# Optimization experiments

Measured on AMD Instinct MI355X. Metric: run time of the kernel, lower is better.

Reference implementation:

```python
import jax, jax.numpy as jnp
import numpy as np

D_MODEL = 1024
NUM_HEADS = 16

def setup_inputs() -> dict:
    key = jax.random.key(0)
    ks = jax.random.split(key, 5)
    std = np.sqrt(2.0 / (D_MODEL + D_MODEL))
    def w(k):
        # trunc_normal approx: normal clipped to +-3 std
        v = jax.random.truncated_normal(k, -3.0, 3.0, (D_MODEL, D_MODEL), dtype=jnp.float32) * std
        return v
    return {
        "x": jax.random.normal(ks[0], (2, 2048, D_MODEL), dtype=jnp.float32),
        "w_q": w(ks[1]),
        "w_k": w(ks[2]),
        "w_v": w(ks[3]),
        "w_o": w(ks[4]),
    }

def reference(x, w_q, w_k, w_v, w_o):
    B, S, D = x.shape
    H = NUM_HEADS
    dk = D // H
    # Linear: y = x @ W^T  (weight is [d_out, d_in])
    def proj(w):
        y = jnp.einsum('bsd,ed->bse', x, w)
        return y.reshape(B, S, H, dk).transpose(0, 2, 1, 3)  # [B,H,S,dk]
    q, k, v = proj(w_q), proj(w_k), proj(w_v)
    scale = 1.0 / jnp.sqrt(jnp.float32(dk))
    scores = jnp.einsum('bhqd,bhkd->bhqk', q, k) * scale  # [B,H,S,S]
    causal = jnp.tril(jnp.ones((S, S), dtype=bool))
    scores = jnp.where(causal, scores, -jnp.inf)
    attn = jax.nn.softmax(scores, axis=-1)
    out = jnp.einsum('bhqk,bhkd->bhqd', attn, v)  # [B,H,S,dk]
    out = out.transpose(0, 2, 1, 3).reshape(B, S, D)
    return jnp.einsum('bsd,ed->bse', out, w_o)
```

## Files before the change

kernel.cpp:

```cpp
#include <hip/hip_runtime.h>
#include <hip/hip_bf16.h>
#include <stdint.h>

#define S_LEN 2048
#define DM    1024
#define NH    16
#define DK    64
#define NBATCH 2

typedef __attribute__((ext_vector_type(8))) short bf8_t;
typedef __attribute__((ext_vector_type(4))) short s4_t;
typedef __attribute__((ext_vector_type(4))) float f4_t;

using bf16 = __hip_bfloat16;

#define NEG_BIG (-1.0e30f)
#define SCALE2  (0.125f * 1.44269504088896f)

static __device__ __forceinline__ f4_t mfma16(bf8_t a, bf8_t b, f4_t c) {
    return __builtin_amdgcn_mfma_f32_16x16x32_bf16(a, b, c, 0, 0, 0);
}

static __device__ __forceinline__ short f2b(float f) {
    __hip_bfloat16 h = __float2bfloat16(f);
    return *reinterpret_cast<short*>(&h);
}

static __device__ __forceinline__ void g2l16(const bf16* g, bf16* l) {
#if __has_builtin(__builtin_amdgcn_global_load_lds)
    __builtin_amdgcn_global_load_lds(
        (const __attribute__((address_space(1))) void*)g,
        (__attribute__((address_space(3))) void*)l, 16, 0, 0);
#else
    *(bf8_t*)l = *(const bf8_t*)g;
#endif
}

__global__ __launch_bounds__(256)
void cvt_all(const float* __restrict__ x,  const float* __restrict__ wq,
             const float* __restrict__ wk, const float* __restrict__ wv,
             const float* __restrict__ wo, bf16* __restrict__ ob) {
    const size_t SEG = 1u << 20;
    size_t i = ((size_t)blockIdx.x * 256 + threadIdx.x) * 8;
    const float* src;
    if      (i < 4 * SEG) src = x  + i;
    else if (i < 5 * SEG) src = wq + (i - 4 * SEG);
    else if (i < 6 * SEG) src = wk + (i - 5 * SEG);
    else if (i < 7 * SEG) src = wv + (i - 6 * SEG);
    else                  src = wo + (i - 7 * SEG);
    float4 f0 = *(const float4*)(src);
    float4 f1 = *(const float4*)(src + 4);
    bf8_t v;
    v[0]=f2b(f0.x); v[1]=f2b(f0.y); v[2]=f2b(f0.z); v[3]=f2b(f0.w);
    v[4]=f2b(f1.x); v[5]=f2b(f1.y); v[6]=f2b(f1.z); v[7]=f2b(f1.w);
    *(bf8_t*)(ob + i) = v;
}

#define GEMM_B_MAINLOOP(Aptr, Bptr)                                          \
    __shared__ bf16 As[128][32];                                             \
    __shared__ bf16 Bs[128][32];                                             \
    const int tid  = threadIdx.x;                                            \
    const int lane = tid & 63;                                               \
    const int w    = tid >> 6;                                               \
    const int wr   = w >> 1, wc = w & 1;                                     \
    const int lhi  = lane >> 4, llo = lane & 15;                             \
    const int bm   = blockIdx.x * 128;                                       \
    const int bn   = blockIdx.y * 128;                                       \
    const int r0c  = tid >> 2;                           \
    const int c0c  = (tid & 3) << 3;                     \
    const int r1c  = (256 + tid) >> 2;                                       \
    f4_t acc[4][4] = {};                                                     \
    for (int k0 = 0; k0 < 1024; k0 += 32) {                                  \
        __syncthreads();                                                     \
        g2l16(Aptr + (size_t)(bm + r0c) * 1024 + k0 + c0c,                   \
              &As[0][0] + (size_t)tid * 8);                                  \
        g2l16(Aptr + (size_t)(bm + r1c) * 1024 + k0 + c0c,                   \
              &As[0][0] + (size_t)(256 + tid) * 8);                          \
        g2l16(Bptr + (size_t)(bn + r0c) * 1024 + k0 + c0c,                   \
              &Bs[0][0] + (size_t)tid * 8);                                  \
        g2l16(Bptr + (size_t)(bn + r1c) * 1024 + k0 + c0c,                   \
              &Bs[0][0] + (size_t)(256 + tid) * 8);                          \
        asm volatile("s_waitcnt vmcnt(0)" ::: "memory");                     \
        __syncthreads();                                                     \
        bf8_t af[4], bfr[4];                                                 \
        _Pragma("unroll")                                                    \
        for (int i = 0; i < 4; ++i) {                                        \
            af[i]  = *(const bf8_t*)(&As[wr * 64 + i * 16 + llo][lhi * 8]);  \
            bfr[i] = *(const bf8_t*)(&Bs[wc * 64 + i * 16 + llo][lhi * 8]);  \
        }                                                                    \
        _Pragma("unroll")                                                    \
        for (int mi = 0; mi < 4; ++mi)                                       \
            _Pragma("unroll")                                                \
            for (int ni = 0; ni < 4; ++ni)                                   \
                acc[mi][ni] = mfma16(af[mi], bfr[ni], acc[mi][ni]);          \
    }

__global__ __launch_bounds__(256)
void gemm_qkv_b(const bf16* __restrict__ xb,
                const bf16* __restrict__ wqb, const bf16* __restrict__ wkb,
                const bf16* __restrict__ wvb,
                bf16* __restrict__ qws, bf16* __restrict__ kws,
                bf16* __restrict__ vtws) {
    const int z = blockIdx.z;
    const bf16* Wb = (z == 0) ? wqb : (z == 1) ? wkb : wvb;
    GEMM_B_MAINLOOP(xb, Wb)

    if (z < 2) {
        bf16* C = z ? kws : qws;
        const float sc = z ? 1.0f : SCALE2;
        #pragma unroll
        for (int mi = 0; mi < 4; ++mi)
            #pragma unroll
            for (int ni = 0; ni < 4; ++ni)
                #pragma unroll
                for (int r = 0; r < 4; ++r) {
                    int m = bm + wr * 64 + mi * 16 + lhi * 4 + r;
                    int n = bn + wc * 64 + ni * 16 + llo;
                    int b = m >> 11, s = m & (S_LEN - 1);
                    int h = n >> 6,  d = n & (DK - 1);
                    C[(((size_t)(b * NH + h) * S_LEN) + s) * DK + d] =
                        __float2bfloat16(acc[mi][ni][r] * sc);
                }
    } else {
        #pragma unroll
        for (int mi = 0; mi < 4; ++mi)
            #pragma unroll
            for (int ni = 0; ni < 4; ++ni) {
                int m0 = bm + wr * 64 + mi * 16 + lhi * 4;
                int n  = bn + wc * 64 + ni * 16 + llo;
                int b = m0 >> 11, s0 = m0 & (S_LEN - 1);
                int h = n >> 6,   d  = n & (DK - 1);
                s4_t pk;
                #pragma unroll
                for (int r = 0; r < 4; ++r) pk[r] = f2b(acc[mi][ni][r]);
                *(s4_t*)&vtws[(((size_t)(b * NH + h) * DK) + d) * S_LEN + s0] = pk;
            }
    }
}

__global__ __launch_bounds__(256)
void gemm_o_b(const bf16* __restrict__ A, const bf16* __restrict__ Wb,
              float* __restrict__ C) {
    GEMM_B_MAINLOOP(A, Wb)
    #pragma unroll
    for (int mi = 0; mi < 4; ++mi)
        #pragma unroll
        for (int ni = 0; ni < 4; ++ni)
            #pragma unroll
            for (int r = 0; r < 4; ++r) {
                int m = bm + wr * 64 + mi * 16 + lhi * 4 + r;
                int n = bn + wc * 64 + ni * 16 + llo;
                C[(size_t)m * DM + n] = acc[mi][ni][r];
            }
}

__global__ __launch_bounds__(256)
void gemm_qkv_f32(const float* __restrict__ x,
                  const float* __restrict__ wqp, const float* __restrict__ wkp,
                  const float* __restrict__ wvp,
                  bf16* __restrict__ qws, bf16* __restrict__ kws,
                  bf16* __restrict__ vtws) {
    constexpr int K = DM;
    constexpr int BM = 128, BK = 32, LDT = BK + 8;
    const int z = blockIdx.z;
    const float* W = (z == 0) ? wqp : (z == 1) ? wkp : wvp;
    __shared__ bf16 As[BM][LDT];
    __shared__ bf16 Bs[BM][LDT];
    const int tid  = threadIdx.x;
    const int lane = tid & 63;
    const int w    = tid >> 6;
    const int wr   = w >> 1, wc = w & 1;
    const int lhi  = lane >> 4, llo = lane & 15;
    const int bm   = blockIdx.x * BM;
    const int bn   = blockIdx.y * BM;
    f4_t acc[4][4] = {};
    for (int k0 = 0; k0 < K; k0 += BK) {
        __syncthreads();
        #pragma unroll
        for (int t = 0; t < 2; ++t) {
            int c   = t * 256 + tid;
            int row = c >> 2;
            int col = (c & 3) << 3;
            {
                const float* s0 = x + (size_t)(bm + row) * K + k0 + col;
                float4 f0 = *(const float4*)(s0);
                float4 f1 = *(const float4*)(s0 + 4);
                bf8_t a8;
                a8[0]=f2b(f0.x); a8[1]=f2b(f0.y); a8[2]=f2b(f0.z); a8[3]=f2b(f0.w);
                a8[4]=f2b(f1.x); a8[5]=f2b(f1.y); a8[6]=f2b(f1.z); a8[7]=f2b(f1.w);
                *(bf8_t*)(&As[row][col]) = a8;
            }
            {
                const float* s0 = W + (size_t)(bn + row) * K + k0 + col;
                float4 f0 = *(const float4*)(s0);
                float4 f1 = *(const float4*)(s0 + 4);
                bf8_t b8;
                b8[0]=f2b(f0.x); b8[1]=f2b(f0.y); b8[2]=f2b(f0.z); b8[3]=f2b(f0.w);
                b8[4]=f2b(f1.x); b8[5]=f2b(f1.y); b8[6]=f2b(f1.z); b8[7]=f2b(f1.w);
                *(bf8_t*)(&Bs[row][col]) = b8;
            }
        }
        __syncthreads();
        bf8_t af[4], bfr[4];
        #pragma unroll
        for (int i = 0; i < 4; ++i) {
            af[i]  = *(const bf8_t*)(&As[wr * 64 + i * 16 + llo][lhi * 8]);
            bfr[i] = *(const bf8_t*)(&Bs[wc * 64 + i * 16 + llo][lhi * 8]);
        }
        #pragma unroll
        for (int mi = 0; mi < 4; ++mi)
            #pragma unroll
            for (int ni = 0; ni < 4; ++ni)
                acc[mi][ni] = mfma16(af[mi], bfr[ni], acc[mi][ni]);
    }
    if (z < 2) {
        bf16* C = z ? kws : qws;
        const float sc = z ? 1.0f : SCALE2;
        #pragma unroll
        for (int mi = 0; mi < 4; ++mi)
            #pragma unroll
            for (int ni = 0; ni < 4; ++ni)
                #pragma unroll
                for (int r = 0; r < 4; ++r) {
                    int m = bm + wr * 64 + mi * 16 + lhi * 4 + r;
                    int n = bn + wc * 64 + ni * 16 + llo;
                    int b = m >> 11, s = m & (S_LEN - 1);
                    int h = n >> 6,  d = n & (DK - 1);
                    C[(((size_t)(b * NH + h) * S_LEN) + s) * DK + d] =
                        __float2bfloat16(acc[mi][ni][r] * sc);
                }
    } else {
        #pragma unroll
        for (int mi = 0; mi < 4; ++mi)
            #pragma unroll
            for (int ni = 0; ni < 4; ++ni) {
                int m0 = bm + wr * 64 + mi * 16 + lhi * 4;
                int n  = bn + wc * 64 + ni * 16 + llo;
                int b = m0 >> 11, s0 = m0 & (S_LEN - 1);
                int h = n >> 6,   d  = n & (DK - 1);
                s4_t pk;
                #pragma unroll
                for (int r = 0; r < 4; ++r) pk[r] = f2b(acc[mi][ni][r]);
                *(s4_t*)&vtws[(((size_t)(b * NH + h) * DK) + d) * S_LEN + s0] = pk;
            }
    }
}

__global__ __launch_bounds__(256)
void gemm_o_f32(const bf16* __restrict__ A, const float* __restrict__ W,
                float* __restrict__ C) {
    constexpr int N = DM;
    constexpr int K = DM;
    constexpr int BM = 128, BN = 64, BK = 32, LDT = BK + 8;
    __shared__ bf16 As[BM][LDT];
    __shared__ bf16 Bs[BN][LDT];
    const int tid  = threadIdx.x;
    const int lane = tid & 63;
    const int w    = tid >> 6;
    const int wr   = w >> 1, wc = w & 1;
    const int lhi  = lane >> 4, llo = lane & 15;
    const int bm   = blockIdx.x * BM;
    const int bn   = blockIdx.y * BN;
    f4_t acc[4][2] = {};
    for (int k0 = 0; k0 < K; k0 += BK) {
        __syncthreads();
        #pragma unroll
        for (int t = 0; t < 2; ++t) {
            int c   = t * 256 + tid;
            int row = c >> 2;
            int col = (c & 3) << 3;
            *(bf8_t*)(&As[row][col]) =
                *(const bf8_t*)(A + (size_t)(bm + row) * K + k0 + col);
        }
        {
            int row = tid >> 2;
            int col = (tid & 3) << 3;
            const float* s0 = W + (size_t)(bn + row) * K + k0 + col;
            float4 f0 = *(const float4*)(s0);
            float4 f1 = *(const float4*)(s0 + 4);
            bf8_t b8;
            b8[0]=f2b(f0.x); b8[1]=f2b(f0.y); b8[2]=f2b(f0.z); b8[3]=f2b(f0.w);
            b8[4]=f2b(f1.x); b8[5]=f2b(f1.y); b8[6]=f2b(f1.z); b8[7]=f2b(f1.w);
            *(bf8_t*)(&Bs[row][col]) = b8;
        }
        __syncthreads();
        bf8_t af[4], bfr[2];
        #pragma unroll
        for (int i = 0; i < 4; ++i)
            af[i] = *(const bf8_t*)(&As[wr * 64 + i * 16 + llo][lhi * 8]);
        #pragma unroll
        for (int i = 0; i < 2; ++i)
            bfr[i] = *(const bf8_t*)(&Bs[wc * 32 + i * 16 + llo][lhi * 8]);
        #pragma unroll
        for (int mi = 0; mi < 4; ++mi)
            #pragma unroll
            for (int ni = 0; ni < 2; ++ni)
                acc[mi][ni] = mfma16(af[mi], bfr[ni], acc[mi][ni]);
    }
    #pragma unroll
    for (int mi = 0; mi < 4; ++mi)
        #pragma unroll
        for (int ni = 0; ni < 2; ++ni)
            #pragma unroll
            for (int r = 0; r < 4; ++r) {
                int m = bm + wr * 64 + mi * 16 + lhi * 4 + r;
                int n = bn + wc * 32 + ni * 16 + llo;
                C[(size_t)m * N + n] = acc[mi][ni][r];
            }
}

__global__ __launch_bounds__(256, 3)
void attn_fwd(const bf16* __restrict__ Q, const bf16* __restrict__ K,
              const bf16* __restrict__ Vt, bf16* __restrict__ AO) {
    __shared__ bf16 Ks[2][64][72];
    __shared__ bf16 Vs[2][64][72];
    __shared__ bf16 Pl[4][16][72];

    const int bh = blockIdx.x;
    const int qt = 31 - (int)blockIdx.y;
    const int q0 = qt * 64;
    const int nt = qt + 1;

    const bf16* Qh = Q  + (size_t)bh * S_LEN * DK;
    const bf16* Kh = K  + (size_t)bh * S_LEN * DK;
    const bf16* Vh = Vt + (size_t)bh * DK * S_LEN;

    const int tid  = threadIdx.x;
    const int lane = tid & 63;
    const int w    = tid >> 6;
    const int lhi  = lane >> 4, llo = lane & 15;
    const int r0   = tid >> 3;
    const int scol = (tid & 7) << 3;

    const bf16* qrow = Qh + (size_t)(q0 + w * 16 + llo) * DK;
    const bf8_t qf0 = *(const bf8_t*)(qrow + lhi * 8);
    const bf8_t qf1 = *(const bf8_t*)(qrow + 32 + lhi * 8);

    bf8_t ones;
    #pragma unroll
    for (int j = 0; j < 8; ++j) ones[j] = (short)0x3F80;

    *(bf8_t*)&Ks[0][r0][scol]      = *(const bf8_t*)(Kh + (size_t)r0 * DK + scol);
    *(bf8_t*)&Ks[0][r0 + 32][scol] = *(const bf8_t*)(Kh + (size_t)(r0 + 32) * DK + scol);
    *(bf8_t*)&Vs[0][r0][scol]      = *(const bf8_t*)(Vh + (size_t)r0 * S_LEN + scol);
    *(bf8_t*)&Vs[0][r0 + 32][scol] = *(const bf8_t*)(Vh + (size_t)(r0 + 32) * S_LEN + scol);
    __syncthreads();

    f4_t o[4] = {};
    float lr[4] = {0.f, 0.f, 0.f, 0.f};
    float mr = NEG_BIG;

    bf8_t kr0, kr1, vr0, vr1;

    for (int t = 0; t < nt; ++t) {
        const int kv0 = t * 64;
        const int cur = t & 1;

        if (t + 1 < nt) {
            kr0 = *(const bf8_t*)(Kh + (size_t)(kv0 + 64 + r0) * DK + scol);
            kr1 = *(const bf8_t*)(Kh + (size_t)(kv0 + 96 + r0) * DK + scol);
            vr0 = *(const bf8_t*)(Vh + (size_t)r0 * S_LEN + kv0 + 64 + scol);
            vr1 = *(const bf8_t*)(Vh + (size_t)(r0 + 32) * S_LEN + kv0 + 64 + scol);
        }

        f4_t s[4] = {};
        __builtin_amdgcn_s_setprio(1);
        #pragma unroll
        for (int nf = 0; nf < 4; ++nf) {
            bf8_t k0f = *(const bf8_t*)&Ks[cur][nf * 16 + llo][lhi * 8];
            bf8_t k1f = *(const bf8_t*)&Ks[cur][nf * 16 + llo][32 + lhi * 8];
            s[nf] = mfma16(k0f, qf0, s[nf]);
            s[nf] = mfma16(k1f, qf1, s[nf]);
        }
        __builtin_amdgcn_s_setprio(0);

        if (kv0 == q0) {
            const int qloc = w * 16 + llo;
            #pragma unroll
            for (int nf = 0; nf < 4; ++nf)
                #pragma unroll
                for (int r = 0; r < 4; ++r)
                    if (nf * 16 + lhi * 4 + r > qloc) s[nf][r] = NEG_BIG;
        }

        float pm = s[0][0];
        #pragma unroll
        for (int nf = 0; nf < 4; ++nf)
            #pragma unroll
            for (int r = 0; r < 4; ++r) pm = fmaxf(pm, s[nf][r]);
        pm = fmaxf(pm, __shfl_xor(pm, 16));
        pm = fmaxf(pm, __shfl_xor(pm, 32));

        float mn = fmaxf(mr, pm);
        float alpha = exp2f(mr - mn);
        mr = mn;

        #pragma unroll
        for (int nf = 0; nf < 4; ++nf) {
            s4_t pk;
            #pragma unroll
            for (int r = 0; r < 4; ++r) pk[r] = f2b(exp2f(s[nf][r] - mr));
            *(s4_t*)&Pl[w][llo][nf * 16 + lhi * 4] = pk;
        }

        float alpha_o[4];
        #pragma unroll
        for (int r = 0; r < 4; ++r) alpha_o[r] = __shfl(alpha, lhi * 4 + r);
        #pragma unroll
        for (int df = 0; df < 4; ++df)
            #pragma unroll
            for (int r = 0; r < 4; ++r) o[df][r] *= alpha_o[r];

        asm volatile("s_waitcnt lgkmcnt(0)" ::: "memory");
        __builtin_amdgcn_sched_barrier(0);

        bf8_t pa0 = *(const bf8_t*)&Pl[w][llo][lhi * 8];
        bf8_t pa1 = *(const bf8_t*)&Pl[w][llo][32 + lhi * 8];

        f4_t rsacc = {};
        rsacc = mfma16(pa0, ones, rsacc);
        rsacc = mfma16(pa1, ones, rsacc);

        __builtin_amdgcn_s_setprio(1);
        #pragma unroll
        for (int df = 0; df < 4; ++df) {
            bf8_t vb0 = *(const bf8_t*)&Vs[cur][df * 16 + llo][lhi * 8];
            bf8_t vb1 = *(const bf8_t*)&Vs[cur][df * 16 + llo][32 + lhi * 8];
            o[df] = mfma16(pa0, vb0, o[df]);
            o[df] = mfma16(pa1, vb1, o[df]);
        }
        __builtin_amdgcn_s_setprio(0);

        #pragma unroll
        for (int r = 0; r < 4; ++r) lr[r] = lr[r] * alpha_o[r] + rsacc[r];

        if (t + 1 < nt) {
            *(bf8_t*)&Ks[cur ^ 1][r0][scol]      = kr0;
            *(bf8_t*)&Ks[cur ^ 1][r0 + 32][scol] = kr1;
            *(bf8_t*)&Vs[cur ^ 1][r0][scol]      = vr0;
            *(bf8_t*)&Vs[cur ^ 1][r0 + 32][scol] = vr1;
        }
        __syncthreads();
    }

    const int b = bh >> 4, h = bh & (NH - 1);
    #pragma unroll
    for (int r = 0; r < 4; ++r) {
        float inv = 1.0f / lr[r];
        int q = q0 + w * 16 + lhi * 4 + r;
        bf16* orow = AO + ((size_t)(b * S_LEN + q) * DM) + h * DK;
        #pragma unroll
        for (int df = 0; df < 4; ++df)
            orow[df * 16 + llo] = __float2bfloat16(o[df][r] * inv);
    }
}

extern "C" void kernel_launch(void* const* d_in, const int* in_sizes, int n_in,
                              void* d_out, int out_size, void* d_ws, size_t ws_size,
                              hipStream_t stream) {
    const float* x  = (const float*)d_in[0];
    const float* wq = (const float*)d_in[1];
    const float* wk = (const float*)d_in[2];
    const float* wv = (const float*)d_in[3];
    const float* wo = (const float*)d_in[4];
    float* out = (float*)d_out;

    const size_t SEG   = 1u << 20;
    const size_t elems = 4 * SEG;
    const size_t need_fast = (8 * SEG + 3 * elems) * sizeof(bf16);

    dim3 blk(256);

    if (ws_size >= need_fast) {
        bf16* ob   = (bf16*)d_ws;
        bf16* xb   = ob;
        bf16* wqb  = ob + 4 * SEG;
        bf16* wkb  = ob + 5 * SEG;
        bf16* wvb  = ob + 6 * SEG;
        bf16* wob  = ob + 7 * SEG;
        bf16* qws  = ob + 8 * SEG;
        bf16* kws  = qws + elems;
        bf16* vtws = kws + elems;
        bf16* aws  = xb;

        cvt_all<<<4096, blk, 0, stream>>>(x, wq, wk, wv, wo, ob);
        gemm_qkv_b<<<dim3(32, 8, 3), blk, 0, stream>>>(xb, wqb, wkb, wvb,
                                                       qws, kws, vtws);
        attn_fwd<<<dim3(NBATCH * NH, 32), blk, 0, stream>>>(qws, kws, vtws, aws);
        gemm_o_b<<<dim3(32, 8), blk, 0, stream>>>(aws, wob, out);
    } else {
        if (ws_size < elems * 4 * sizeof(bf16)) return;
        bf16* qws  = (bf16*)d_ws;
        bf16* kws  = qws + elems;
        bf16* vtws = kws + elems;
        bf16* aws  = vtws + elems;

        gemm_qkv_f32<<<dim3(32, 8, 3), blk, 0, stream>>>(x, wq, wk, wv,
                                                         qws, kws, vtws);
        attn_fwd<<<dim3(NBATCH * NH, 32), blk, 0, stream>>>(qws, kws, vtws, aws);
        gemm_o_f32<<<dim3(32, 16), blk, 0, stream>>>(aws, wo, out);
    }
}
```

Before: 117.8 us.

## Use 128-row query tiles with 512 threads and direct global-to-LDS swizzled loads

The attention kernel now processes 128 query rows per block with 8 waves, so each K/V tile is shared by twice as many queries. K/V tiles are loaded with direct global-to-LDS copies (g2l16) into an XOR-swizzled, unpadded layout instead of staging through registers. Waves whose 16 rows lie entirely before a key tile skip that tile's compute. This halves K/V reloads and frees staging registers, but it adds a vmcnt wait before every barrier and gives per-wave causal imbalance within a block.

```diff
diff --git a/kernel.cpp b/kernel.cpp
--- a/kernel.cpp
+++ b/kernel.cpp
@@ -309,17 +309,17 @@
             }
 }
 
-__global__ __launch_bounds__(256, 3)
+__global__ __launch_bounds__(512, 4)
 void attn_fwd(const bf16* __restrict__ Q, const bf16* __restrict__ K,
               const bf16* __restrict__ Vt, bf16* __restrict__ AO) {
-    __shared__ bf16 Ks[2][64][72];
-    __shared__ bf16 Vs[2][64][72];
-    __shared__ bf16 Pl[4][16][72];
+    __shared__ bf16 Ks[2][64][64];
+    __shared__ bf16 Vs[2][64][64];
+    __shared__ bf16 Pl[8][16][72];
 
     const int bh = blockIdx.x;
-    const int qt = 31 - (int)blockIdx.y;
-    const int q0 = qt * 64;
-    const int nt = qt + 1;
+    const int qt = 15 - (int)blockIdx.y;
+    const int q0 = qt * 128;
+    const int nt = 2 * qt + 2;
 
     const bf16* Qh = Q  + (size_t)bh * S_LEN * DK;
     const bf16* Kh = K  + (size_t)bh * S_LEN * DK;
@@ -329,8 +329,11 @@
     const int lane = tid & 63;
     const int w    = tid >> 6;
     const int lhi  = lane >> 4, llo = lane & 15;
-    const int r0   = tid >> 3;
-    const int scol = (tid & 7) << 3;
+    const int qw   = q0 + w * 16;
+    const int sw   = llo & 7;
+
+    const int srow = tid >> 3;
+    const int schk = (tid & 7) ^ (srow & 7);
 
     const bf16* qrow = Qh + (size_t)(q0 + w * 16 + llo) * DK;
     const bf8_t qf0 = *(const bf8_t*)(qrow + lhi * 8);
@@ -340,106 +343,102 @@
     #pragma unroll
     for (int j = 0; j < 8; ++j) ones[j] = (short)0x3F80;
 
-    *(bf8_t*)&Ks[0][r0][scol]      = *(const bf8_t*)(Kh + (size_t)r0 * DK + scol);
-    *(bf8_t*)&Ks[0][r0 + 32][scol] = *(const bf8_t*)(Kh + (size_t)(r0 + 32) * DK + scol);
-    *(bf8_t*)&Vs[0][r0][scol]      = *(const bf8_t*)(Vh + (size_t)r0 * S_LEN + scol);
-    *(bf8_t*)&Vs[0][r0 + 32][scol] = *(const bf8_t*)(Vh + (size_t)(r0 + 32) * S_LEN + scol);
+    g2l16(Kh + (size_t)srow * DK + schk * 8, &Ks[0][0][0] + (size_t)tid * 8);
+    g2l16(Vh + (size_t)srow * S_LEN + schk * 8, &Vs[0][0][0] + (size_t)tid * 8);
+    asm volatile("s_waitcnt vmcnt(0)" ::: "memory");
     __syncthreads();
 
     f4_t o[4] = {};
     float lr[4] = {0.f, 0.f, 0.f, 0.f};
     float mr = NEG_BIG;
 
-    bf8_t kr0, kr1, vr0, vr1;
-
     for (int t = 0; t < nt; ++t) {
         const int kv0 = t * 64;
         const int cur = t & 1;
 
         if (t + 1 < nt) {
-            kr0 = *(const bf8_t*)(Kh + (size_t)(kv0 + 64 + r0) * DK + scol);
-            kr1 = *(const bf8_t*)(Kh + (size_t)(kv0 + 96 + r0) * DK + scol);
-            vr0 = *(const bf8_t*)(Vh + (size_t)r0 * S_LEN + kv0 + 64 + scol);
-            vr1 = *(const bf8_t*)(Vh + (size_t)(r0 + 32) * S_LEN + kv0 + 64 + scol);
+            g2l16(Kh + (size_t)(kv0 + 64 + srow) * DK + schk * 8,
+                  &Ks[cur ^ 1][0][0] + (size_t)tid * 8);
+            g2l16(Vh + (size_t)srow * S_LEN + kv0 + 64 + schk * 8,
+                  &Vs[cur ^ 1][0][0] + (size_t)tid * 8);
         }
 
-        f4_t s[4] = {};
-        __builtin_amdgcn_s_setprio(1);
-        #pragma unroll
-        for (int nf = 0; nf < 4; ++nf) {
-            bf8_t k0f = *(const bf8_t*)&Ks[cur][nf * 16 + llo][lhi * 8];
-            bf8_t k1f = *(const bf8_t*)&Ks[cur][nf * 16 + llo][32 + lhi * 8];
-            s[nf] = mfma16(k0f, qf0, s[nf]);
-            s[nf] = mfma16(k1f, qf1, s[nf]);
+        if (kv0 <= qw + 15) {
+            f4_t s[4] = {};
+            __builtin_amdgcn_s_setprio(1);
+            #pragma unroll
+            for (int nf = 0; nf < 4; ++nf) {
+                const int R = nf * 16 + llo;
+                bf8_t k0f = *(const bf8_t*)&Ks[cur][R][(lhi ^ sw) * 8];
+                bf8_t k1f = *(const bf8_t*)&Ks[cur][R][((4 + lhi) ^ sw) * 8];
+                s[nf] = mfma16(k0f, qf0, s[nf]);
+                s[nf] = mfma16(k1f, qf1, s[nf]);
+            }
+            __builtin_amdgcn_s_setprio(0);
+
+            if (kv0 + 63 > qw) {
+                #pragma unroll
+                for (int nf = 0; nf < 4; ++nf)
+                    #pragma unroll
+                    for (int r = 0; r < 4; ++r)
+                        if (kv0 + nf * 16 + lhi * 4 + r > qw + llo)
+                            s[nf][r] = NEG_BIG;
+            }
+
+            float pm = s[0][0];
+            #pragma unroll
+            for (int nf = 0; nf < 4; ++nf)
+                #pragma unroll
+                for (int r = 0; r < 4; ++r) pm = fmaxf(pm, s[nf][r]);
+            pm = fmaxf(pm, __shfl_xor(pm, 16));
+            pm = fmaxf(pm, __shfl_xor(pm, 32));
+
+            float mn = fmaxf(mr, pm);
+            float alpha = exp2f(mr - mn);
+            mr = mn;
+
+            #pragma unroll
+            for (int nf = 0; nf < 4; ++nf) {
+                s4_t pk;
+                #pragma unroll
+                for (int r = 0; r < 4; ++r) pk[r] = f2b(exp2f(s[nf][r] - mr));
+                *(s4_t*)&Pl[w][llo][nf * 16 + lhi * 4] = pk;
+            }
+
+            float alpha_o[4];
+            #pragma unroll
+            for (int r = 0; r < 4; ++r) alpha_o[r] = __shfl(alpha, lhi * 4 + r);
+            #pragma unroll
+            for (int df = 0; df < 4; ++df)
+                #pragma unroll
+                for (int r = 0; r < 4; ++r) o[df][r] *= alpha_o[r];
+
+            asm volatile("s_waitcnt lgkmcnt(0)" ::: "memory");
+            __builtin_amdgcn_sched_barrier(0);
+
+            bf8_t pa0 = *(const bf8_t*)&Pl[w][llo][lhi * 8];
+            bf8_t pa1 = *(const bf8_t*)&Pl[w][llo][32 + lhi * 8];
+
+            f4_t rsacc = {};
+            rsacc = mfma16(pa0, ones, rsacc);
+            rsacc = mfma16(pa1, ones, rsacc);
+
+            __builtin_amdgcn_s_setprio(1);
+            #pragma unroll
+            for (int df = 0; df < 4; ++df) {
+                const int R = df * 16 + llo;
+                bf8_t vb0 = *(const bf8_t*)&Vs[cur][R][(lhi ^ sw) * 8];
+                bf8_t vb1 = *(const bf8_t*)&Vs[cur][R][((4 + lhi) ^ sw) * 8];
+                o[df] = mfma16(pa0, vb0, o[df]);
+                o[df] = mfma16(pa1, vb1, o[df]);
+            }
+            __builtin_amdgcn_s_setprio(0);
+
+            #pragma unroll
+            for (int r = 0; r < 4; ++r) lr[r] = lr[r] * alpha_o[r] + rsacc[r];
         }
-        __builtin_amdgcn_s_setprio(0);
-
-        if (kv0 == q0) {
-            const int qloc = w * 16 + llo;
-            #pragma unroll
-            for (int nf = 0; nf < 4; ++nf)
-                #pragma unroll
-                for (int r = 0; r < 4; ++r)
-                    if (nf * 16 + lhi * 4 + r > qloc) s[nf][r] = NEG_BIG;
-        }
-
-        float pm = s[0][0];
-        #pragma unroll
-        for (int nf = 0; nf < 4; ++nf)
-            #pragma unroll
-            for (int r = 0; r < 4; ++r) pm = fmaxf(pm, s[nf][r]);
-        pm = fmaxf(pm, __shfl_xor(pm, 16));
-        pm = fmaxf(pm, __shfl_xor(pm, 32));
-
-        float mn = fmaxf(mr, pm);
-        float alpha = exp2f(mr - mn);
-        mr = mn;
-
-        #pragma unroll
-        for (int nf = 0; nf < 4; ++nf) {
-            s4_t pk;
-            #pragma unroll
-            for (int r = 0; r < 4; ++r) pk[r] = f2b(exp2f(s[nf][r] - mr));
-            *(s4_t*)&Pl[w][llo][nf * 16 + lhi * 4] = pk;
-        }
-
-        float alpha_o[4];
-        #pragma unroll
-        for (int r = 0; r < 4; ++r) alpha_o[r] = __shfl(alpha, lhi * 4 + r);
-        #pragma unroll
-        for (int df = 0; df < 4; ++df)
-            #pragma unroll
-            for (int r = 0; r < 4; ++r) o[df][r] *= alpha_o[r];
-
-        asm volatile("s_waitcnt lgkmcnt(0)" ::: "memory");
-        __builtin_amdgcn_sched_barrier(0);
-
-        bf8_t pa0 = *(const bf8_t*)&Pl[w][llo][lhi * 8];
-        bf8_t pa1 = *(const bf8_t*)&Pl[w][llo][32 + lhi * 8];
-
-        f4_t rsacc = {};
-        rsacc = mfma16(pa0, ones, rsacc);
-        rsacc = mfma16(pa1, ones, rsacc);
-
-        __builtin_amdgcn_s_setprio(1);
-        #pragma unroll
-        for (int df = 0; df < 4; ++df) {
-            bf8_t vb0 = *(const bf8_t*)&Vs[cur][df * 16 + llo][lhi * 8];
-            bf8_t vb1 = *(const bf8_t*)&Vs[cur][df * 16 + llo][32 + lhi * 8];
-            o[df] = mfma16(pa0, vb0, o[df]);
-            o[df] = mfma16(pa1, vb1, o[df]);
-        }
-        __builtin_amdgcn_s_setprio(0);
-
-        #pragma unroll
-        for (int r = 0; r < 4; ++r) lr[r] = lr[r] * alpha_o[r] + rsacc[r];
-
-        if (t + 1 < nt) {
-            *(bf8_t*)&Ks[cur ^ 1][r0][scol]      = kr0;
-            *(bf8_t*)&Ks[cur ^ 1][r0 + 32][scol] = kr1;
-            *(bf8_t*)&Vs[cur ^ 1][r0][scol]      = vr0;
-            *(bf8_t*)&Vs[cur ^ 1][r0 + 32][scol] = vr1;
-        }
+
+        asm volatile("s_waitcnt vmcnt(0)" ::: "memory");
         __syncthreads();
     }
 
@@ -486,7 +485,7 @@
         cvt_all<<<4096, blk, 0, stream>>>(x, wq, wk, wv, wo, ob);
         gemm_qkv_b<<<dim3(32, 8, 3), blk, 0, stream>>>(xb, wqb, wkb, wvb,
                                                        qws, kws, vtws);
-        attn_fwd<<<dim3(NBATCH * NH, 32), blk, 0, stream>>>(qws, kws, vtws, aws);
+        attn_fwd<<<dim3(NBATCH * NH, 16), dim3(512), 0, stream>>>(qws, kws, vtws, aws);
         gemm_o_b<<<dim3(32, 8), blk, 0, stream>>>(aws, wob, out);
     } else {
         if (ws_size < elems * 4 * sizeof(bf16)) return;
@@ -497,7 +496,7 @@
 
         gemm_qkv_f32<<<dim3(32, 8, 3), blk, 0, stream>>>(x, wq, wk, wv,
                                                          qws, kws, vtws);
-        attn_fwd<<<dim3(NBATCH * NH, 32), blk, 0, stream>>>(qws, kws, vtws, aws);
+        attn_fwd<<<dim3(NBATCH * NH, 16), dim3(512), 0, stream>>>(qws, kws, vtws, aws);
         gemm_o_f32<<<dim3(32, 16), blk, 0, stream>>>(aws, wo, out);
     }
 }
```

Measured after the change: 120.8 us. 2.5% more time.
